# Kernel tuning notes

Measured on AMD Instinct MI355X. Metric: run time of the kernel, lower is better.

## Reference

```python
import jax, jax.numpy as jnp
import numpy as np

N_NODES = 100000
N_GRAPHS = 64


def _gcn_norm(edge_index, num_nodes):
    # Add self-loops and compute symmetric normalization (PyG GCNConv gcn_norm).
    src = jnp.concatenate([edge_index[0], jnp.arange(num_nodes, dtype=edge_index.dtype)])
    dst = jnp.concatenate([edge_index[1], jnp.arange(num_nodes, dtype=edge_index.dtype)])
    deg = jax.ops.segment_sum(jnp.ones_like(dst, dtype=jnp.float32), dst, num_segments=num_nodes)
    dinv = jnp.where(deg > 0, jax.lax.rsqrt(deg), 0.0)
    norm = dinv[src] * dinv[dst]  # [E + N]
    return src, dst, norm


def _gcn_conv(x, src, dst, norm, W, b, num_nodes):
    h = x @ W                                   # [N, out]
    msg = h[src] * norm[:, None]                # gather + scale  [E+N, out]
    out = jax.ops.segment_sum(msg, dst, num_segments=num_nodes)  # scatter-add
    return out + b


def setup_inputs() -> dict:
    key = jax.random.key(0)
    ks = jax.random.split(key, 8)
    E = 1600000
    pos = jax.random.normal(ks[0], (N_NODES, 3), dtype=jnp.float32)
    edge_index = jax.random.randint(ks[1], (2, E), 0, N_NODES, dtype=jnp.int64)
    batch = jnp.sort(jax.random.randint(ks[2], (N_NODES,), 0, N_GRAPHS, dtype=jnp.int64))
    def glorot(k, shape):
        lim = np.sqrt(6.0 / (shape[0] + shape[1])).astype(np.float32)
        return jax.random.uniform(k, shape, dtype=jnp.float32, minval=-lim, maxval=lim)
    return {
        "pos": pos,
        "edge_index": edge_index,
        "batch": batch,
        "W1": glorot(ks[3], (3, 64)),  "b1": jnp.zeros((64,), jnp.float32),
        "W2": glorot(ks[4], (64, 64)), "b2": jnp.zeros((64,), jnp.float32),
        "W3": glorot(ks[5], (64, 24)), "b3": jnp.zeros((24,), jnp.float32),
    }


def reference(pos, edge_index, batch, W1, b1, W2, b2, W3, b3):
    src, dst, norm = _gcn_norm(edge_index, N_NODES)
    h = jax.nn.relu(_gcn_conv(pos, src, dst, norm, W1, b1, N_NODES))
    h = jax.nn.relu(_gcn_conv(h, src, dst, norm, W2, b2, N_NODES))
    y = _gcn_conv(h, src, dst, norm, W3, b3, N_NODES)  # [N, 24]
    # global_mean_pool over batch ids, then tanh
    sums = jax.ops.segment_sum(y, batch, num_segments=N_GRAPHS)          # [G, 24]
    counts = jax.ops.segment_sum(jnp.ones((N_NODES,), jnp.float32), batch, num_segments=N_GRAPHS)
    mean = sums / jnp.maximum(counts, 1.0)[:, None]
    return jnp.tanh(mean)
```

## Files before the change

### kernel.cpp

```cpp
#include <hip/hip_runtime.h>
#include <math.h>

#define NNODES 100000
#define NGRAPHS 64
#define NB 391


__device__ __forceinline__ unsigned int f2bf(float x) {
    union { float f; unsigned int u; } v;
    v.f = x;
    unsigned int r = v.u + 0x7FFFu + ((v.u >> 16) & 1u);
    return r >> 16;
}
__device__ __forceinline__ unsigned int pack2bf(float lo, float hi) {
    return f2bf(lo) | (f2bf(hi) << 16);
}
__device__ __forceinline__ float bflo(unsigned int u) {
    union { unsigned int u; float f; } v;
    v.u = u << 16;
    return v.f;
}
__device__ __forceinline__ float bfhi(unsigned int u) {
    union { unsigned int u; float f; } v;
    v.u = u & 0xFFFF0000u;
    return v.f;
}


__global__ void bucket_count(const int* __restrict__ dst, int* __restrict__ bucketCnt, int E) {
    __shared__ int h[NB];
    for (int k = threadIdx.x; k < NB; k += 256) h[k] = 0;
    __syncthreads();
    int base = blockIdx.x * 2048 + threadIdx.x;
#pragma unroll
    for (int k = 0; k < 8; ++k) {
        int e = base + k * 256;
        if (e < E) atomicAdd(&h[dst[e] >> 8], 1);
    }
    __syncthreads();
    for (int k = threadIdx.x; k < NB; k += 256)
        if (h[k]) atomicAdd(&bucketCnt[k], h[k]);
}

__global__ void bucket_scan(const int* __restrict__ bucketCnt, int* __restrict__ bucketBase,
                            int* __restrict__ bucketCur, int E) {
    __shared__ int lds[512];
    int tid = threadIdx.x;
    lds[tid] = (tid < NB) ? bucketCnt[tid] : 0;
    __syncthreads();
    for (int off = 1; off < 512; off <<= 1) {
        int v = (tid >= off) ? lds[tid - off] : 0;
        __syncthreads();
        lds[tid] += v;
        __syncthreads();
    }
    int excl = (tid > 0) ? lds[tid - 1] : 0;
    if (tid < NB) {
        bucketBase[tid] = excl;
        bucketCur[tid] = excl;
    }
    if (tid == NB) bucketBase[NB] = excl;
}

__global__ void bucket_scatter(const int* __restrict__ src, const int* __restrict__ dst,
                               int* __restrict__ bucketCur, unsigned int* __restrict__ packed,
                               int E) {
    __shared__ int h[NB];
    __shared__ int cur[NB];
    for (int k = threadIdx.x; k < NB; k += 256) h[k] = 0;
    __syncthreads();
    int base = blockIdx.x * 2048 + threadIdx.x;
    int d[8], s[8], b[8];
#pragma unroll
    for (int k = 0; k < 8; ++k) {
        int e = base + k * 256;
        if (e < E) {
            d[k] = dst[e];
            s[k] = src[e];
            b[k] = d[k] >> 8;
            atomicAdd(&h[b[k]], 1);
        }
    }
    __syncthreads();
    for (int k = threadIdx.x; k < NB; k += 256) {
        int c = h[k];
        cur[k] = c ? atomicAdd(&bucketCur[k], c) : 0;
    }
    __syncthreads();
#pragma unroll
    for (int k = 0; k < 8; ++k) {
        int e = base + k * 256;
        if (e < E) {
            int pos = atomicAdd(&cur[b[k]], 1);
            packed[pos] = ((unsigned int)(d[k] & 255) << 17) | (unsigned int)s[k];
        }
    }
}

__global__ void bucket_build(const unsigned int* __restrict__ packed,
                             const int* __restrict__ bucketBase, int* __restrict__ rowptr,
                             int* __restrict__ col, float* __restrict__ dinv, int N_, int E) {
    __shared__ int cnt[256];
    __shared__ int bas[256];
    int tid = threadIdx.x;
    int b = blockIdx.x;
    int beg = bucketBase[b], end = bucketBase[b + 1];
    cnt[tid] = 0;
    __syncthreads();
    for (int k = beg + tid; k < end; k += 256) atomicAdd(&cnt[packed[k] >> 17], 1);
    __syncthreads();
    int myCnt = cnt[tid];
    bas[tid] = myCnt;
    __syncthreads();
    for (int off = 1; off < 256; off <<= 1) {
        int v = (tid >= off) ? bas[tid - off] : 0;
        __syncthreads();
        bas[tid] += v;
        __syncthreads();
    }
    int excl = beg + ((tid > 0) ? bas[tid - 1] : 0);
    int node = (b << 8) + tid;
    if (node <= N_) rowptr[node] = excl;
    if (node < N_) dinv[node] = rsqrtf((float)myCnt + 1.0f);
    __syncthreads();
    bas[tid] = excl;
    __syncthreads();
    for (int k = beg + tid; k < end; k += 256) {
        unsigned int p = packed[k];
        int pos = atomicAdd(&bas[p >> 17], 1);
        col[pos] = (int)(p & 0x1FFFFu);
    }
}


__global__ void pad_pos(const float* __restrict__ pos, float4* __restrict__ p4, int n) {
    int i = blockIdx.x * blockDim.x + threadIdx.x;
    if (i < n) {
        float4 v;
        v.x = pos[i * 3 + 0];
        v.y = pos[i * 3 + 1];
        v.z = pos[i * 3 + 2];
        v.w = 0.0f;
        p4[i] = v;
    }
}


__global__ void gather_pos(const int* __restrict__ rowptr, const int* __restrict__ col,
                           const float4* __restrict__ p4, const float* __restrict__ dinv,
                           float4* __restrict__ outp, int n) {
    int i = blockIdx.x * blockDim.x + threadIdx.x;
    if (i >= n) return;
    float di = dinv[i];
    int beg = rowptr[i];
    int end = rowptr[i + 1];
    float4 sv = p4[i];
    float ax0 = sv.x * di, ay0 = sv.y * di, az0 = sv.z * di;
    float ax1 = 0, ay1 = 0, az1 = 0;
    float ax2 = 0, ay2 = 0, az2 = 0;
    float ax3 = 0, ay3 = 0, az3 = 0;
    int j = beg;
    for (; j + 4 <= end; j += 4) {
        int s0 = col[j], s1 = col[j + 1], s2 = col[j + 2], s3 = col[j + 3];
        float w0 = dinv[s0], w1 = dinv[s1], w2 = dinv[s2], w3 = dinv[s3];
        float4 v0 = p4[s0], v1 = p4[s1], v2 = p4[s2], v3 = p4[s3];
        ax0 += v0.x * w0; ay0 += v0.y * w0; az0 += v0.z * w0;
        ax1 += v1.x * w1; ay1 += v1.y * w1; az1 += v1.z * w1;
        ax2 += v2.x * w2; ay2 += v2.y * w2; az2 += v2.z * w2;
        ax3 += v3.x * w3; ay3 += v3.y * w3; az3 += v3.z * w3;
    }
    for (; j < end; ++j) {
        int s = col[j];
        float w = dinv[s];
        float4 v = p4[s];
        ax1 += v.x * w; ay1 += v.y * w; az1 += v.z * w;
    }
    float4 o;
    o.x = di * ((ax0 + ax1) + (ax2 + ax3));
    o.y = di * ((ay0 + ay1) + (ay2 + ay3));
    o.z = di * ((az0 + az1) + (az2 + az3));
    o.w = 0.0f;
    outp[i] = o;
}

__global__ void mm1_fused(const float4* __restrict__ aggP, const float* __restrict__ W1,
                          const float* __restrict__ b1, float* __restrict__ out, int n) {
    int t = blockIdx.x * blockDim.x + threadIdx.x;
    if (t >= n * 64) return;
    int i = t >> 6;
    int f = t & 63;
    float4 x = aggP[i];
    float acc = b1[f] + x.x * W1[f] + x.y * W1[64 + f] + x.z * W1[128 + f];
    out[t] = fmaxf(acc, 0.0f);
}


template <int F4, int TY>
__global__ void mm_tiled_b16(const float4* __restrict__ x4, const float* __restrict__ W,
                             uint2* __restrict__ outb, int n) {
    constexpr int ROWS = TY * 4;
    __shared__ float xs[ROWS][65];
    __shared__ float4 ws[64 * F4];
    const int tid = threadIdx.x;
    const int rowBase = blockIdx.x * ROWS;
    const int BT = F4 * TY;

    for (int idx = tid; idx < ROWS * 16; idx += BT) {
        int r = idx >> 4;
        int k4 = idx & 15;
        int gr = rowBase + r;
        float4 v = (gr < n) ? x4[(size_t)gr * 16 + k4] : make_float4(0, 0, 0, 0);
        xs[r][k4 * 4 + 0] = v.x;
        xs[r][k4 * 4 + 1] = v.y;
        xs[r][k4 * 4 + 2] = v.z;
        xs[r][k4 * 4 + 3] = v.w;
    }
    const float4* W4 = (const float4*)W;
    for (int idx = tid; idx < 64 * F4; idx += BT) ws[idx] = W4[idx];
    __syncthreads();

    const int f4 = tid % F4;
    const int r0 = (tid / F4) * 4;
    float4 a0 = make_float4(0, 0, 0, 0), a1 = a0, a2 = a0, a3 = a0;
#pragma unroll 4
    for (int k = 0; k < 64; ++k) {
        float4 wv = ws[k * F4 + f4];
        float xa = xs[r0 + 0][k];
        float xb = xs[r0 + 1][k];
        float xc = xs[r0 + 2][k];
        float xd = xs[r0 + 3][k];
        a0.x += wv.x * xa; a0.y += wv.y * xa; a0.z += wv.z * xa; a0.w += wv.w * xa;
        a1.x += wv.x * xb; a1.y += wv.y * xb; a1.z += wv.z * xb; a1.w += wv.w * xb;
        a2.x += wv.x * xc; a2.y += wv.y * xc; a2.z += wv.z * xc; a2.w += wv.w * xc;
        a3.x += wv.x * xd; a3.y += wv.y * xd; a3.z += wv.z * xd; a3.w += wv.w * xd;
    }
    if (rowBase + r0 + 0 < n)
        outb[(size_t)(rowBase + r0 + 0) * F4 + f4] = make_uint2(pack2bf(a0.x, a0.y), pack2bf(a0.z, a0.w));
    if (rowBase + r0 + 1 < n)
        outb[(size_t)(rowBase + r0 + 1) * F4 + f4] = make_uint2(pack2bf(a1.x, a1.y), pack2bf(a1.z, a1.w));
    if (rowBase + r0 + 2 < n)
        outb[(size_t)(rowBase + r0 + 2) * F4 + f4] = make_uint2(pack2bf(a2.x, a2.y), pack2bf(a2.z, a2.w));
    if (rowBase + r0 + 3 < n)
        outb[(size_t)(rowBase + r0 + 3) * F4 + f4] = make_uint2(pack2bf(a3.x, a3.y), pack2bf(a3.z, a3.w));
}


template <int C8, bool RELU, bool BIAS>
__global__ void gather_b16(const int* __restrict__ rowptr, const int* __restrict__ col,
                           const uint4* __restrict__ h, const float* __restrict__ dinv,
                           const float* __restrict__ bias, float4* __restrict__ out, int n) {
    int t = blockIdx.x * blockDim.x + threadIdx.x;
    if (t >= n * C8) return;
    int i = t / C8;
    int c8 = t - i * C8;
    float di = dinv[i];
    int beg = rowptr[i];
    int end = rowptr[i + 1];

    float acc[8];
    {
        uint4 sv = h[(size_t)i * C8 + c8];
        acc[0] = bflo(sv.x) * di; acc[1] = bfhi(sv.x) * di;
        acc[2] = bflo(sv.y) * di; acc[3] = bfhi(sv.y) * di;
        acc[4] = bflo(sv.z) * di; acc[5] = bfhi(sv.z) * di;
        acc[6] = bflo(sv.w) * di; acc[7] = bfhi(sv.w) * di;
    }
    int j = beg;
    for (; j + 8 <= end; j += 8) {
        int s[8];
        float w[8];
        uint4 v[8];
#pragma unroll
        for (int k = 0; k < 8; ++k) s[k] = col[j + k];
#pragma unroll
        for (int k = 0; k < 8; ++k) {
            v[k] = h[(size_t)s[k] * C8 + c8];
            w[k] = dinv[s[k]];
        }
#pragma unroll
        for (int k = 0; k < 8; ++k) {
            acc[0] += bflo(v[k].x) * w[k]; acc[1] += bfhi(v[k].x) * w[k];
            acc[2] += bflo(v[k].y) * w[k]; acc[3] += bfhi(v[k].y) * w[k];
            acc[4] += bflo(v[k].z) * w[k]; acc[5] += bfhi(v[k].z) * w[k];
            acc[6] += bflo(v[k].w) * w[k]; acc[7] += bfhi(v[k].w) * w[k];
        }
    }
    for (; j + 4 <= end; j += 4) {
        int s[4];
        float w[4];
        uint4 v[4];
#pragma unroll
        for (int k = 0; k < 4; ++k) s[k] = col[j + k];
#pragma unroll
        for (int k = 0; k < 4; ++k) {
            v[k] = h[(size_t)s[k] * C8 + c8];
            w[k] = dinv[s[k]];
        }
#pragma unroll
        for (int k = 0; k < 4; ++k) {
            acc[0] += bflo(v[k].x) * w[k]; acc[1] += bfhi(v[k].x) * w[k];
            acc[2] += bflo(v[k].y) * w[k]; acc[3] += bfhi(v[k].y) * w[k];
            acc[4] += bflo(v[k].z) * w[k]; acc[5] += bfhi(v[k].z) * w[k];
            acc[6] += bflo(v[k].w) * w[k]; acc[7] += bfhi(v[k].w) * w[k];
        }
    }
    for (; j < end; ++j) {
        int s = col[j];
        float w = dinv[s];
        uint4 v = h[(size_t)s * C8 + c8];
        acc[0] += bflo(v.x) * w; acc[1] += bfhi(v.x) * w;
        acc[2] += bflo(v.y) * w; acc[3] += bfhi(v.y) * w;
        acc[4] += bflo(v.z) * w; acc[5] += bfhi(v.z) * w;
        acc[6] += bflo(v.w) * w; acc[7] += bfhi(v.w) * w;
    }
#pragma unroll
    for (int k = 0; k < 8; ++k) acc[k] *= di;
    if (BIAS) {
        const float* bv = bias + c8 * 8;
#pragma unroll
        for (int k = 0; k < 8; ++k) acc[k] += bv[k];
    }
    if (RELU) {
#pragma unroll
        for (int k = 0; k < 8; ++k) acc[k] = fmaxf(acc[k], 0.0f);
    }
    float4 o0 = make_float4(acc[0], acc[1], acc[2], acc[3]);
    float4 o1 = make_float4(acc[4], acc[5], acc[6], acc[7]);
    out[(size_t)t * 2 + 0] = o0;
    out[(size_t)t * 2 + 1] = o1;
}


__global__ void pool_reduce(const float* __restrict__ y, const int* __restrict__ batch,
                            float* __restrict__ sums, float* __restrict__ cnt, int n) {
    __shared__ float ls[NGRAPHS * 24];
    __shared__ float lc[NGRAPHS];
    for (int k = threadIdx.x; k < NGRAPHS * 24; k += blockDim.x) ls[k] = 0.0f;
    for (int k = threadIdx.x; k < NGRAPHS; k += blockDim.x) lc[k] = 0.0f;
    __syncthreads();
    int total = n * 24;
    int stride = gridDim.x * blockDim.x;
    for (int t = blockIdx.x * blockDim.x + threadIdx.x; t < total; t += stride) {
        int i = t / 24;
        int c = t - i * 24;
        atomicAdd(&ls[batch[i] * 24 + c], y[t]);
    }
    for (int i = blockIdx.x * blockDim.x + threadIdx.x; i < n; i += stride) {
        atomicAdd(&lc[batch[i]], 1.0f);
    }
    __syncthreads();
    for (int k = threadIdx.x; k < NGRAPHS * 24; k += blockDim.x)
        if (ls[k] != 0.0f) atomicAdd(&sums[k], ls[k]);
    for (int k = threadIdx.x; k < NGRAPHS; k += blockDim.x)
        if (lc[k] != 0.0f) atomicAdd(&cnt[k], lc[k]);
}

__global__ void pool_finish(const float* __restrict__ sums, const float* __restrict__ cnt,
                            const float* __restrict__ b3, float* __restrict__ out) {
    int t = blockIdx.x * blockDim.x + threadIdx.x;
    if (t >= NGRAPHS * 24) return;
    int g = t / 24;
    int c = t - g * 24;
    float m = sums[t] / fmaxf(cnt[g], 1.0f) + b3[c];
    out[t] = tanhf(m);
}


static inline int gridFor(long long total, int block) {
    return (int)((total + block - 1) / block);
}

extern "C" void kernel_launch(void* const* d_in, const int* in_sizes, int n_in,
                              void* d_out, int out_size, void* d_ws, size_t ws_size,
                              hipStream_t stream) {
    const float* pos   = (const float*)d_in[0];
    const int*   ei    = (const int*)d_in[1];
    const int*   batch = (const int*)d_in[2];
    const float* W1    = (const float*)d_in[3];
    const float* b1    = (const float*)d_in[4];
    const float* W2    = (const float*)d_in[5];
    const float* b2    = (const float*)d_in[6];
    const float* W3    = (const float*)d_in[7];
    const float* b3    = (const float*)d_in[8];
    float*       out   = (float*)d_out;

    const int N = NNODES;
    const int E = in_sizes[1] / 2;
    const int* src = ei;
    const int* dst = ei + E;

    char* p = (char*)d_ws;
    float4* pos4   = (float4*)p;        p += (size_t)N * sizeof(float4);
    float4* aggP   = (float4*)p;        p += (size_t)N * sizeof(float4);
    float*  bufA   = (float*)p;         p += (size_t)N * 64 * sizeof(float);
    unsigned int* bufB = (unsigned int*)p;  p += (size_t)N * 32 * sizeof(unsigned int);
    float*  bufY   = (float*)p;         p += (size_t)N * 24 * sizeof(float);
    float*  dinv   = (float*)p;         p += (size_t)N * sizeof(float);
    float*  pool   = (float*)p;         p += (size_t)NGRAPHS * 24 * sizeof(float);
    float*  cnt    = (float*)p;         p += (size_t)NGRAPHS * sizeof(float);
    int*    rowptr = (int*)p;           p += (size_t)(N + 1) * sizeof(int);
    int*    bCnt   = (int*)p;           p += (NB + 1) * sizeof(int);
    int*    bBase  = (int*)p;           p += (NB + 1) * sizeof(int);
    int*    bCur   = (int*)p;           p += (NB + 1) * sizeof(int);
    unsigned int* packed = (unsigned int*)p;  p += (size_t)E * sizeof(unsigned int);
    int*    col    = (int*)p;           p += (size_t)E * sizeof(int);

    const int B = 256;
    const int edgeBlocks = gridFor(E, 2048);

    hipMemsetAsync(bCnt, 0, (NB + 1) * sizeof(int), stream);
    bucket_count<<<edgeBlocks, 256, 0, stream>>>(dst, bCnt, E);
    bucket_scan<<<1, 512, 0, stream>>>(bCnt, bBase, bCur, E);
    bucket_scatter<<<edgeBlocks, 256, 0, stream>>>(src, dst, bCur, packed, E);
    bucket_build<<<NB, 256, 0, stream>>>(packed, bBase, rowptr, col, dinv, N, E);

    pad_pos<<<gridFor(N, B), B, 0, stream>>>(pos, pos4, N);
    gather_pos<<<gridFor(N, B), B, 0, stream>>>(rowptr, col, pos4, dinv, aggP, N);
    mm1_fused<<<gridFor((long long)N * 64, B), B, 0, stream>>>(aggP, W1, b1, bufA, N);

    mm_tiled_b16<16, 16><<<gridFor(N, 64), 256, 0, stream>>>(
        (const float4*)bufA, W2, (uint2*)bufB, N);
    gather_b16<8, true, true><<<gridFor((long long)N * 8, B), B, 0, stream>>>(
        rowptr, col, (const uint4*)bufB, dinv, b2, (float4*)bufA, N);

    mm_tiled_b16<6, 32><<<gridFor(N, 128), 192, 0, stream>>>(
        (const float4*)bufA, W3, (uint2*)bufB, N);
    gather_b16<3, false, false><<<gridFor((long long)N * 3, B), B, 0, stream>>>(
        rowptr, col, (const uint4*)bufB, dinv, (const float*)nullptr, (float4*)bufY, N);

    hipMemsetAsync(pool, 0, (size_t)(NGRAPHS * 24 + NGRAPHS) * sizeof(float), stream);
    pool_reduce<<<256, 256, 0, stream>>>(bufY, batch, pool, cnt, N);
    pool_finish<<<gridFor(NGRAPHS * 24, B), B, 0, stream>>>(pool, cnt, b3, out);
}
```

Measured before the change: 317.7 us.

## Fuse GCN stages: drop pos padding, fuse mm1+mm2, bf16 intermediates, fuse gather3 with pooling

Several kernels are removed or fused. gather_pos now reads pos directly instead of a padded copy. The layer-1 linear+ReLU is computed in shared memory inside the W2 matmul kernel. The layer-2 gather writes bf16 output, which mm3 reads. The final gather accumulates straight into per-block pooled partials, which pool_finish reduces, so the bufY write/read, a memset and the pool_reduce kernel go away. This cuts launches and global memory traffic, at the cost of extra bf16 rounding on h2 and a serial 304-step reduction in pool_finish.

```diff
diff --git a/kernel.cpp b/kernel.cpp
--- a/kernel.cpp
+++ b/kernel.cpp
@@ -4,6 +4,7 @@
 #define NNODES 100000
 #define NGRAPHS 64
 #define NB 391
+#define NBLK3 304
 
 
 __device__ __forceinline__ unsigned int f2bf(float x) {
@@ -133,47 +134,31 @@
 }
 
 
-__global__ void pad_pos(const float* __restrict__ pos, float4* __restrict__ p4, int n) {
-    int i = blockIdx.x * blockDim.x + threadIdx.x;
-    if (i < n) {
-        float4 v;
-        v.x = pos[i * 3 + 0];
-        v.y = pos[i * 3 + 1];
-        v.z = pos[i * 3 + 2];
-        v.w = 0.0f;
-        p4[i] = v;
-    }
-}
-
-
 __global__ void gather_pos(const int* __restrict__ rowptr, const int* __restrict__ col,
-                           const float4* __restrict__ p4, const float* __restrict__ dinv,
+                           const float* __restrict__ pos, const float* __restrict__ dinv,
                            float4* __restrict__ outp, int n) {
     int i = blockIdx.x * blockDim.x + threadIdx.x;
     if (i >= n) return;
     float di = dinv[i];
     int beg = rowptr[i];
     int end = rowptr[i + 1];
-    float4 sv = p4[i];
-    float ax0 = sv.x * di, ay0 = sv.y * di, az0 = sv.z * di;
+    float ax0 = pos[i * 3 + 0] * di, ay0 = pos[i * 3 + 1] * di, az0 = pos[i * 3 + 2] * di;
     float ax1 = 0, ay1 = 0, az1 = 0;
     float ax2 = 0, ay2 = 0, az2 = 0;
     float ax3 = 0, ay3 = 0, az3 = 0;
     int j = beg;
     for (; j + 4 <= end; j += 4) {
-        int s0 = col[j], s1 = col[j + 1], s2 = col[j + 2], s3 = col[j + 3];
-        float w0 = dinv[s0], w1 = dinv[s1], w2 = dinv[s2], w3 = dinv[s3];
-        float4 v0 = p4[s0], v1 = p4[s1], v2 = p4[s2], v3 = p4[s3];
-        ax0 += v0.x * w0; ay0 += v0.y * w0; az0 += v0.z * w0;
-        ax1 += v1.x * w1; ay1 += v1.y * w1; az1 += v1.z * w1;
-        ax2 += v2.x * w2; ay2 += v2.y * w2; az2 += v2.z * w2;
-        ax3 += v3.x * w3; ay3 += v3.y * w3; az3 += v3.z * w3;
+        int s0 = col[j] * 3, s1 = col[j + 1] * 3, s2 = col[j + 2] * 3, s3 = col[j + 3] * 3;
+        float w0 = dinv[col[j]], w1 = dinv[col[j + 1]], w2 = dinv[col[j + 2]], w3 = dinv[col[j + 3]];
+        ax0 += pos[s0] * w0; ay0 += pos[s0 + 1] * w0; az0 += pos[s0 + 2] * w0;
+        ax1 += pos[s1] * w1; ay1 += pos[s1 + 1] * w1; az1 += pos[s1 + 2] * w1;
+        ax2 += pos[s2] * w2; ay2 += pos[s2 + 1] * w2; az2 += pos[s2 + 2] * w2;
+        ax3 += pos[s3] * w3; ay3 += pos[s3 + 1] * w3; az3 += pos[s3 + 2] * w3;
     }
     for (; j < end; ++j) {
         int s = col[j];
         float w = dinv[s];
-        float4 v = p4[s];
-        ax1 += v.x * w; ay1 += v.y * w; az1 += v.z * w;
+        ax1 += pos[s * 3] * w; ay1 += pos[s * 3 + 1] * w; az1 += pos[s * 3 + 2] * w;
     }
     float4 o;
     o.x = di * ((ax0 + ax1) + (ax2 + ax3));
@@ -183,48 +168,38 @@
     outp[i] = o;
 }
 
-__global__ void mm1_fused(const float4* __restrict__ aggP, const float* __restrict__ W1,
-                          const float* __restrict__ b1, float* __restrict__ out, int n) {
-    int t = blockIdx.x * blockDim.x + threadIdx.x;
-    if (t >= n * 64) return;
-    int i = t >> 6;
-    int f = t & 63;
-    float4 x = aggP[i];
-    float acc = b1[f] + x.x * W1[f] + x.y * W1[64 + f] + x.z * W1[128 + f];
-    out[t] = fmaxf(acc, 0.0f);
-}
-
-
-template <int F4, int TY>
-__global__ void mm_tiled_b16(const float4* __restrict__ x4, const float* __restrict__ W,
-                             uint2* __restrict__ outb, int n) {
-    constexpr int ROWS = TY * 4;
-    __shared__ float xs[ROWS][65];
-    __shared__ float4 ws[64 * F4];
+
+__global__ void mm12_fused(const float4* __restrict__ aggP, const float* __restrict__ W1,
+                           const float* __restrict__ b1, const float* __restrict__ W2,
+                           uint2* __restrict__ outb, int n) {
+    __shared__ float4 ap[64];
+    __shared__ float xs[64][65];
+    __shared__ float4 ws[64 * 16];
     const int tid = threadIdx.x;
-    const int rowBase = blockIdx.x * ROWS;
-    const int BT = F4 * TY;
-
-    for (int idx = tid; idx < ROWS * 16; idx += BT) {
-        int r = idx >> 4;
-        int k4 = idx & 15;
-        int gr = rowBase + r;
-        float4 v = (gr < n) ? x4[(size_t)gr * 16 + k4] : make_float4(0, 0, 0, 0);
-        xs[r][k4 * 4 + 0] = v.x;
-        xs[r][k4 * 4 + 1] = v.y;
-        xs[r][k4 * 4 + 2] = v.z;
-        xs[r][k4 * 4 + 3] = v.w;
-    }
-    const float4* W4 = (const float4*)W;
-    for (int idx = tid; idx < 64 * F4; idx += BT) ws[idx] = W4[idx];
-    __syncthreads();
-
-    const int f4 = tid % F4;
-    const int r0 = (tid / F4) * 4;
+    const int rowBase = blockIdx.x * 64;
+
+    if (tid < 64) {
+        int gr = rowBase + tid;
+        ap[tid] = (gr < n) ? aggP[gr] : make_float4(0, 0, 0, 0);
+    }
+    const float4* W24 = (const float4*)W2;
+    for (int idx = tid; idx < 64 * 16; idx += 256) ws[idx] = W24[idx];
+    __syncthreads();
+    for (int idx = tid; idx < 64 * 64; idx += 256) {
+        int r = idx >> 6;
+        int k = idx & 63;
+        float4 a = ap[r];
+        float v = b1[k] + a.x * W1[k] + a.y * W1[64 + k] + a.z * W1[128 + k];
+        xs[r][k] = fmaxf(v, 0.0f);
+    }
+    __syncthreads();
+
+    const int f4 = tid & 15;
+    const int r0 = (tid >> 4) * 4;
     float4 a0 = make_float4(0, 0, 0, 0), a1 = a0, a2 = a0, a3 = a0;
 #pragma unroll 4
     for (int k = 0; k < 64; ++k) {
-        float4 wv = ws[k * F4 + f4];
+        float4 wv = ws[k * 16 + f4];
         float xa = xs[r0 + 0][k];
         float xb = xs[r0 + 1][k];
         float xc = xs[r0 + 2][k];
@@ -235,31 +210,29 @@
         a3.x += wv.x * xd; a3.y += wv.y * xd; a3.z += wv.z * xd; a3.w += wv.w * xd;
     }
     if (rowBase + r0 + 0 < n)
-        outb[(size_t)(rowBase + r0 + 0) * F4 + f4] = make_uint2(pack2bf(a0.x, a0.y), pack2bf(a0.z, a0.w));
+        outb[(size_t)(rowBase + r0 + 0) * 16 + f4] = make_uint2(pack2bf(a0.x, a0.y), pack2bf(a0.z, a0.w));
     if (rowBase + r0 + 1 < n)
-        outb[(size_t)(rowBase + r0 + 1) * F4 + f4] = make_uint2(pack2bf(a1.x, a1.y), pack2bf(a1.z, a1.w));
+        outb[(size_t)(rowBase + r0 + 1) * 16 + f4] = make_uint2(pack2bf(a1.x, a1.y), pack2bf(a1.z, a1.w));
     if (rowBase + r0 + 2 < n)
-        outb[(size_t)(rowBase + r0 + 2) * F4 + f4] = make_uint2(pack2bf(a2.x, a2.y), pack2bf(a2.z, a2.w));
+        outb[(size_t)(rowBase + r0 + 2) * 16 + f4] = make_uint2(pack2bf(a2.x, a2.y), pack2bf(a2.z, a2.w));
     if (rowBase + r0 + 3 < n)
-        outb[(size_t)(rowBase + r0 + 3) * F4 + f4] = make_uint2(pack2bf(a3.x, a3.y), pack2bf(a3.z, a3.w));
-}
-
-
-template <int C8, bool RELU, bool BIAS>
-__global__ void gather_b16(const int* __restrict__ rowptr, const int* __restrict__ col,
-                           const uint4* __restrict__ h, const float* __restrict__ dinv,
-                           const float* __restrict__ bias, float4* __restrict__ out, int n) {
+        outb[(size_t)(rowBase + r0 + 3) * 16 + f4] = make_uint2(pack2bf(a3.x, a3.y), pack2bf(a3.z, a3.w));
+}
+
+
+__global__ void gather2_b16(const int* __restrict__ rowptr, const int* __restrict__ col,
+                            const uint4* __restrict__ h, const float* __restrict__ dinv,
+                            const float* __restrict__ bias, uint4* __restrict__ outb, int n) {
     int t = blockIdx.x * blockDim.x + threadIdx.x;
-    if (t >= n * C8) return;
-    int i = t / C8;
-    int c8 = t - i * C8;
+    if (t >= n * 8) return;
+    int i = t >> 3;
+    int c8 = t & 7;
     float di = dinv[i];
     int beg = rowptr[i];
     int end = rowptr[i + 1];
-
     float acc[8];
     {
-        uint4 sv = h[(size_t)i * C8 + c8];
+        uint4 sv = h[t];
         acc[0] = bflo(sv.x) * di; acc[1] = bfhi(sv.x) * di;
         acc[2] = bflo(sv.y) * di; acc[3] = bfhi(sv.y) * di;
         acc[4] = bflo(sv.z) * di; acc[5] = bfhi(sv.z) * di;
@@ -274,7 +247,7 @@
         for (int k = 0; k < 8; ++k) s[k] = col[j + k];
 #pragma unroll
         for (int k = 0; k < 8; ++k) {
-            v[k] = h[(size_t)s[k] * C8 + c8];
+            v[k] = h[(size_t)s[k] * 8 + c8];
             w[k] = dinv[s[k]];
         }
 #pragma unroll
@@ -285,84 +258,151 @@
             acc[6] += bflo(v[k].w) * w[k]; acc[7] += bfhi(v[k].w) * w[k];
         }
     }
-    for (; j + 4 <= end; j += 4) {
-        int s[4];
-        float w[4];
-        uint4 v[4];
-#pragma unroll
-        for (int k = 0; k < 4; ++k) s[k] = col[j + k];
-#pragma unroll
-        for (int k = 0; k < 4; ++k) {
-            v[k] = h[(size_t)s[k] * C8 + c8];
-            w[k] = dinv[s[k]];
-        }
-#pragma unroll
-        for (int k = 0; k < 4; ++k) {
-            acc[0] += bflo(v[k].x) * w[k]; acc[1] += bfhi(v[k].x) * w[k];
-            acc[2] += bflo(v[k].y) * w[k]; acc[3] += bfhi(v[k].y) * w[k];
-            acc[4] += bflo(v[k].z) * w[k]; acc[5] += bfhi(v[k].z) * w[k];
-            acc[6] += bflo(v[k].w) * w[k]; acc[7] += bfhi(v[k].w) * w[k];
-        }
-    }
     for (; j < end; ++j) {
         int s = col[j];
         float w = dinv[s];
-        uint4 v = h[(size_t)s * C8 + c8];
+        uint4 v = h[(size_t)s * 8 + c8];
         acc[0] += bflo(v.x) * w; acc[1] += bfhi(v.x) * w;
         acc[2] += bflo(v.y) * w; acc[3] += bfhi(v.y) * w;
         acc[4] += bflo(v.z) * w; acc[5] += bfhi(v.z) * w;
         acc[6] += bflo(v.w) * w; acc[7] += bfhi(v.w) * w;
     }
-#pragma unroll
-    for (int k = 0; k < 8; ++k) acc[k] *= di;
-    if (BIAS) {
-        const float* bv = bias + c8 * 8;
-#pragma unroll
-        for (int k = 0; k < 8; ++k) acc[k] += bv[k];
-    }
-    if (RELU) {
-#pragma unroll
-        for (int k = 0; k < 8; ++k) acc[k] = fmaxf(acc[k], 0.0f);
-    }
-    float4 o0 = make_float4(acc[0], acc[1], acc[2], acc[3]);
-    float4 o1 = make_float4(acc[4], acc[5], acc[6], acc[7]);
-    out[(size_t)t * 2 + 0] = o0;
-    out[(size_t)t * 2 + 1] = o1;
-}
-
-
-__global__ void pool_reduce(const float* __restrict__ y, const int* __restrict__ batch,
-                            float* __restrict__ sums, float* __restrict__ cnt, int n) {
-    __shared__ float ls[NGRAPHS * 24];
-    __shared__ float lc[NGRAPHS];
-    for (int k = threadIdx.x; k < NGRAPHS * 24; k += blockDim.x) ls[k] = 0.0f;
-    for (int k = threadIdx.x; k < NGRAPHS; k += blockDim.x) lc[k] = 0.0f;
-    __syncthreads();
-    int total = n * 24;
-    int stride = gridDim.x * blockDim.x;
-    for (int t = blockIdx.x * blockDim.x + threadIdx.x; t < total; t += stride) {
-        int i = t / 24;
-        int c = t - i * 24;
-        atomicAdd(&ls[batch[i] * 24 + c], y[t]);
-    }
-    for (int i = blockIdx.x * blockDim.x + threadIdx.x; i < n; i += stride) {
-        atomicAdd(&lc[batch[i]], 1.0f);
-    }
-    __syncthreads();
-    for (int k = threadIdx.x; k < NGRAPHS * 24; k += blockDim.x)
-        if (ls[k] != 0.0f) atomicAdd(&sums[k], ls[k]);
-    for (int k = threadIdx.x; k < NGRAPHS; k += blockDim.x)
-        if (lc[k] != 0.0f) atomicAdd(&cnt[k], lc[k]);
-}
-
-__global__ void pool_finish(const float* __restrict__ sums, const float* __restrict__ cnt,
+    const float* bv = bias + c8 * 8;
+#pragma unroll
+    for (int k = 0; k < 8; ++k) acc[k] = fmaxf(acc[k] * di + bv[k], 0.0f);
+    outb[t] = make_uint4(pack2bf(acc[0], acc[1]), pack2bf(acc[2], acc[3]),
+                         pack2bf(acc[4], acc[5]), pack2bf(acc[6], acc[7]));
+}
+
+
+__global__ void mm3_b16(const uint4* __restrict__ xb, const float* __restrict__ W,
+                        uint2* __restrict__ outb, int n) {
+    __shared__ float xs[128][65];
+    __shared__ float4 ws[64 * 6];
+    const int tid = threadIdx.x;
+    const int rowBase = blockIdx.x * 128;
+
+    for (int idx = tid; idx < 128 * 8; idx += 192) {
+        int r = idx >> 3;
+        int c8 = idx & 7;
+        int gr = rowBase + r;
+        uint4 v = (gr < n) ? xb[(size_t)gr * 8 + c8] : make_uint4(0, 0, 0, 0);
+        float* xp = &xs[r][c8 * 8];
+        xp[0] = bflo(v.x); xp[1] = bfhi(v.x);
+        xp[2] = bflo(v.y); xp[3] = bfhi(v.y);
+        xp[4] = bflo(v.z); xp[5] = bfhi(v.z);
+        xp[6] = bflo(v.w); xp[7] = bfhi(v.w);
+    }
+    const float4* W4 = (const float4*)W;
+    for (int idx = tid; idx < 64 * 6; idx += 192) ws[idx] = W4[idx];
+    __syncthreads();
+
+    const int f4 = tid % 6;
+    const int r0 = (tid / 6) * 4;
+    float4 a0 = make_float4(0, 0, 0, 0), a1 = a0, a2 = a0, a3 = a0;
+#pragma unroll 4
+    for (int k = 0; k < 64; ++k) {
+        float4 wv = ws[k * 6 + f4];
+        float xa = xs[r0 + 0][k];
+        float xb_ = xs[r0 + 1][k];
+        float xc = xs[r0 + 2][k];
+        float xd = xs[r0 + 3][k];
+        a0.x += wv.x * xa; a0.y += wv.y * xa; a0.z += wv.z * xa; a0.w += wv.w * xa;
+        a1.x += wv.x * xb_; a1.y += wv.y * xb_; a1.z += wv.z * xb_; a1.w += wv.w * xb_;
+        a2.x += wv.x * xc; a2.y += wv.y * xc; a2.z += wv.z * xc; a2.w += wv.w * xc;
+        a3.x += wv.x * xd; a3.y += wv.y * xd; a3.z += wv.z * xd; a3.w += wv.w * xd;
+    }
+    if (rowBase + r0 + 0 < n)
+        outb[(size_t)(rowBase + r0 + 0) * 6 + f4] = make_uint2(pack2bf(a0.x, a0.y), pack2bf(a0.z, a0.w));
+    if (rowBase + r0 + 1 < n)
+        outb[(size_t)(rowBase + r0 + 1) * 6 + f4] = make_uint2(pack2bf(a1.x, a1.y), pack2bf(a1.z, a1.w));
+    if (rowBase + r0 + 2 < n)
+        outb[(size_t)(rowBase + r0 + 2) * 6 + f4] = make_uint2(pack2bf(a2.x, a2.y), pack2bf(a2.z, a2.w));
+    if (rowBase + r0 + 3 < n)
+        outb[(size_t)(rowBase + r0 + 3) * 6 + f4] = make_uint2(pack2bf(a3.x, a3.y), pack2bf(a3.z, a3.w));
+}
+
+
+__global__ void gather3_pool(const int* __restrict__ rowptr, const int* __restrict__ col,
+                             const uint4* __restrict__ h, const float* __restrict__ dinv,
+                             const int* __restrict__ batch, float* __restrict__ partials,
+                             float* __restrict__ cpart, int n) {
+    __shared__ float lpool[NGRAPHS * 24];
+    __shared__ float lcnt[NGRAPHS];
+    for (int k = threadIdx.x; k < NGRAPHS * 24; k += 256) lpool[k] = 0.0f;
+    for (int k = threadIdx.x; k < NGRAPHS; k += 256) lcnt[k] = 0.0f;
+    __syncthreads();
+
+    int total = n * 3;
+    for (int t = blockIdx.x * 256 + threadIdx.x; t < total; t += NBLK3 * 256) {
+        int i = t / 3;
+        int c8 = t - i * 3;
+        float di = dinv[i];
+        int beg = rowptr[i];
+        int end = rowptr[i + 1];
+        float acc[8];
+        {
+            uint4 sv = h[t];
+            acc[0] = bflo(sv.x) * di; acc[1] = bfhi(sv.x) * di;
+            acc[2] = bflo(sv.y) * di; acc[3] = bfhi(sv.y) * di;
+            acc[4] = bflo(sv.z) * di; acc[5] = bfhi(sv.z) * di;
+            acc[6] = bflo(sv.w) * di; acc[7] = bfhi(sv.w) * di;
+        }
+        int j = beg;
+        for (; j + 8 <= end; j += 8) {
+            int s[8];
+            float w[8];
+            uint4 v[8];
+#pragma unroll
+            for (int k = 0; k < 8; ++k) s[k] = col[j + k];
+#pragma unroll
+            for (int k = 0; k < 8; ++k) {
+                v[k] = h[(size_t)s[k] * 3 + c8];
+                w[k] = dinv[s[k]];
+            }
+#pragma unroll
+            for (int k = 0; k < 8; ++k) {
+                acc[0] += bflo(v[k].x) * w[k]; acc[1] += bfhi(v[k].x) * w[k];
+                acc[2] += bflo(v[k].y) * w[k]; acc[3] += bfhi(v[k].y) * w[k];
+                acc[4] += bflo(v[k].z) * w[k]; acc[5] += bfhi(v[k].z) * w[k];
+                acc[6] += bflo(v[k].w) * w[k]; acc[7] += bfhi(v[k].w) * w[k];
+            }
+        }
+        for (; j < end; ++j) {
+            int s = col[j];
+            float w = dinv[s];
+            uint4 v = h[(size_t)s * 3 + c8];
+            acc[0] += bflo(v.x) * w; acc[1] += bfhi(v.x) * w;
+            acc[2] += bflo(v.y) * w; acc[3] += bfhi(v.y) * w;
+            acc[4] += bflo(v.z) * w; acc[5] += bfhi(v.z) * w;
+            acc[6] += bflo(v.w) * w; acc[7] += bfhi(v.w) * w;
+        }
+        int g = batch[i];
+        float* lp = &lpool[g * 24 + c8 * 8];
+#pragma unroll
+        for (int k = 0; k < 8; ++k) atomicAdd(&lp[k], acc[k] * di);
+        if (c8 == 0) atomicAdd(&lcnt[g], 1.0f);
+    }
+    __syncthreads();
+    float* pp = partials + (size_t)blockIdx.x * (NGRAPHS * 24);
+    for (int k = threadIdx.x; k < NGRAPHS * 24; k += 256) pp[k] = lpool[k];
+    float* cp = cpart + (size_t)blockIdx.x * NGRAPHS;
+    for (int k = threadIdx.x; k < NGRAPHS; k += 256) cp[k] = lcnt[k];
+}
+
+__global__ void pool_finish(const float* __restrict__ partials, const float* __restrict__ cpart,
                             const float* __restrict__ b3, float* __restrict__ out) {
     int t = blockIdx.x * blockDim.x + threadIdx.x;
     if (t >= NGRAPHS * 24) return;
     int g = t / 24;
     int c = t - g * 24;
-    float m = sums[t] / fmaxf(cnt[g], 1.0f) + b3[c];
-    out[t] = tanhf(m);
+    float s = 0.0f, cn = 0.0f;
+#pragma unroll 8
+    for (int b = 0; b < NBLK3; ++b) {
+        s += partials[(size_t)b * (NGRAPHS * 24) + t];
+        cn += cpart[(size_t)b * NGRAPHS + g];
+    }
+    out[t] = tanhf(s / fmaxf(cn, 1.0f) + b3[c]);
 }
 
 
@@ -390,14 +430,13 @@
     const int* dst = ei + E;
 
     char* p = (char*)d_ws;
-    float4* pos4   = (float4*)p;        p += (size_t)N * sizeof(float4);
     float4* aggP   = (float4*)p;        p += (size_t)N * sizeof(float4);
-    float*  bufA   = (float*)p;         p += (size_t)N * 64 * sizeof(float);
-    unsigned int* bufB = (unsigned int*)p;  p += (size_t)N * 32 * sizeof(unsigned int);
-    float*  bufY   = (float*)p;         p += (size_t)N * 24 * sizeof(float);
+    uint4*  z2b    = (uint4*)p;         p += (size_t)N * 8 * sizeof(uint4);
+    uint4*  h2b    = (uint4*)p;         p += (size_t)N * 8 * sizeof(uint4);
+    uint4*  y0b    = (uint4*)p;         p += (size_t)N * 3 * sizeof(uint4);
+    float*  partials = (float*)p;       p += (size_t)NBLK3 * NGRAPHS * 24 * sizeof(float);
+    float*  cpart  = (float*)p;         p += (size_t)NBLK3 * NGRAPHS * sizeof(float);
     float*  dinv   = (float*)p;         p += (size_t)N * sizeof(float);
-    float*  pool   = (float*)p;         p += (size_t)NGRAPHS * 24 * sizeof(float);
-    float*  cnt    = (float*)p;         p += (size_t)NGRAPHS * sizeof(float);
     int*    rowptr = (int*)p;           p += (size_t)(N + 1) * sizeof(int);
     int*    bCnt   = (int*)p;           p += (NB + 1) * sizeof(int);
     int*    bBase  = (int*)p;           p += (NB + 1) * sizeof(int);
@@ -414,21 +453,13 @@
     bucket_scatter<<<edgeBlocks, 256, 0, stream>>>(src, dst, bCur, packed, E);
     bucket_build<<<NB, 256, 0, stream>>>(packed, bBase, rowptr, col, dinv, N, E);
 
-    pad_pos<<<gridFor(N, B), B, 0, stream>>>(pos, pos4, N);
-    gather_pos<<<gridFor(N, B), B, 0, stream>>>(rowptr, col, pos4, dinv, aggP, N);
-    mm1_fused<<<gridFor((long long)N * 64, B), B, 0, stream>>>(aggP, W1, b1, bufA, N);
-
-    mm_tiled_b16<16, 16><<<gridFor(N, 64), 256, 0, stream>>>(
-        (const float4*)bufA, W2, (uint2*)bufB, N);
-    gather_b16<8, true, true><<<gridFor((long long)N * 8, B), B, 0, stream>>>(
-        rowptr, col, (const uint4*)bufB, dinv, b2, (float4*)bufA, N);
-
-    mm_tiled_b16<6, 32><<<gridFor(N, 128), 192, 0, stream>>>(
-        (const float4*)bufA, W3, (uint2*)bufB, N);
-    gather_b16<3, false, false><<<gridFor((long long)N * 3, B), B, 0, stream>>>(
-        rowptr, col, (const uint4*)bufB, dinv, (const float*)nullptr, (float4*)bufY, N);
-
-    hipMemsetAsync(pool, 0, (size_t)(NGRAPHS * 24 + NGRAPHS) * sizeof(float), stream);
-    pool_reduce<<<256, 256, 0, stream>>>(bufY, batch, pool, cnt, N);
-    pool_finish<<<gridFor(NGRAPHS * 24, B), B, 0, stream>>>(pool, cnt, b3, out);
-}
+    gather_pos<<<gridFor(N, B), B, 0, stream>>>(rowptr, col, pos, dinv, aggP, N);
+    mm12_fused<<<gridFor(N, 64), 256, 0, stream>>>(aggP, W1, b1, W2, (uint2*)z2b, N);
+
+    gather2_b16<<<gridFor((long long)N * 8, B), B, 0, stream>>>(
+        rowptr, col, z2b, dinv, b2, h2b, N);
+
+    mm3_b16<<<gridFor(N, 128), 192, 0, stream>>>(h2b, W3, (uint2*)y0b, N);
+    gather3_pool<<<NBLK3, 256, 0, stream>>>(rowptr, col, y0b, dinv, batch, partials, cpart, N);
+    pool_finish<<<gridFor(NGRAPHS * 24, B), B, 0, stream>>>(partials, cpart, b3, out);
+}
```

After: 318.6 us. Within noise of the previous version (+0.3%).
